# Kernel optimization log

Measured on AMD Instinct MI355X. Metric: run time of the kernel, lower is better.

The kernel has to match this reference:

```python
import jax, jax.numpy as jnp
import numpy as np

T, B, C = 1024, 16, 1024
H, K, PAD_L = 16, 7, 3  # num_heads, kernel_size, padding_l
OUT = 1024


def setup_inputs() -> dict:
    key = jax.random.key(0)
    ks = jax.random.split(key, 8)
    s_in = 1.0 / np.sqrt(C)
    return {
        "x": jax.random.normal(ks[0], (T, B, C), dtype=jnp.float32),
        "W1": jax.random.normal(ks[1], (C, C), dtype=jnp.float32) * s_in,
        "b1": jnp.zeros((C,), dtype=jnp.float32),
        "Wq": jax.random.normal(ks[2], (C, H * K), dtype=jnp.float32) * s_in,
        "bq": jnp.zeros((H * K,), dtype=jnp.float32),
        "conv_bias": jax.random.normal(ks[3], (C,), dtype=jnp.float32) * 0.02,
        "W2": jax.random.normal(ks[4], (C, OUT), dtype=jnp.float32) * s_in,
        "b2": jnp.zeros((OUT,), dtype=jnp.float32),
    }


def reference(x, W1, b1, Wq, bq, conv_bias, W2, b2):
    # linear1 (glu=False -> no activation)
    h = x @ W1 + b1                       # [T, B, C]
    Tn, Bn, Cn = h.shape
    R = Cn // H                           # channels per head
    # dynamic filter prediction from query (= h), softmax over K taps
    w = (h @ Wq + bq).reshape(Tn, Bn, H, K)
    w = jax.nn.softmax(w, axis=-1)        # [T, B, H, K]
    # unfold1d: pad PAD_L left, K-1-PAD_L right along time, gather K-windows
    hp = jnp.pad(h, ((PAD_L, K - 1 - PAD_L), (0, 0), (0, 0)))
    win = jnp.stack([hp[k:k + Tn] for k in range(K)], axis=-1)  # [T, B, C, K]
    win = win.reshape(Tn, Bn, H, R, K)
    out = jnp.einsum('tbhrk,tbhk->tbhr', win, w).reshape(Tn, Bn, Cn)
    out = out + conv_bias                 # [T, B, C]
    return out @ W2 + b2                  # [T, B, OUT]
```

## Files before the change

kernel.cpp:

```cpp
#include <hip/hip_runtime.h>
#include <math.h>

#define T_DIM 1024
#define B_DIM 16
#define C_DIM 1024
#define H_DIM 16
#define K_TAPS 7
#define PAD_LEFT 3
#define OUT_DIM 1024
#define M_DIM (T_DIM * B_DIM)
#define HK 112
#define HKP 128
#define KD 1024

typedef __attribute__((ext_vector_type(8))) short bf16x8;
typedef __attribute__((ext_vector_type(4))) float f32x4;

__device__ __forceinline__ ushort f2bf(float f) {
    union { float f; unsigned u; } v; v.f = f;
    unsigned u = v.u;
    u += 0x7fffu + ((u >> 16) & 1u);
    return (ushort)(u >> 16);
}
__device__ __forceinline__ float bf2f(ushort h) {
    union { unsigned u; float f; } v; v.u = ((unsigned)h) << 16;
    return v.f;
}

__global__ __launch_bounds__(256) void prep(const float* __restrict__ x,
                                            ushort* __restrict__ xb,
                                            const float* __restrict__ W1s,
                                            const float* __restrict__ Wqs,
                                            const float* __restrict__ W2s,
                                            ushort* __restrict__ W1t,
                                            ushort* __restrict__ Wqt,
                                            ushort* __restrict__ W2t) {
    __shared__ float tile[32][33];
    const int bx = blockIdx.x;
    if (bx < 8192) {
        int i = bx * 256 + threadIdx.x;
        const float4* p = (const float4*)x;
        float4 a = p[2 * i], b = p[2 * i + 1];
        uint4 o;
        o.x = (unsigned)f2bf(a.x) | ((unsigned)f2bf(a.y) << 16);
        o.y = (unsigned)f2bf(a.z) | ((unsigned)f2bf(a.w) << 16);
        o.z = (unsigned)f2bf(b.x) | ((unsigned)f2bf(b.y) << 16);
        o.w = (unsigned)f2bf(b.z) | ((unsigned)f2bf(b.w) << 16);
        ((uint4*)xb)[i] = o;
        return;
    }
    int tb  = bx - 8192;
    int nbx = tb % 68;
    int k0  = (tb / 68) * 32;
    const float* W; ushort* Wt; int N, Npad, nb;
    if (nbx < 32)      { W = W1s; Wt = W1t; N = 1024; Npad = 1024; nb = nbx; }
    else if (nbx < 36) { W = Wqs; Wt = Wqt; N = 112;  Npad = 128;  nb = nbx - 32; }
    else               { W = W2s; Wt = W2t; N = 1024; Npad = 1024; nb = nbx - 36; }
    int n0 = nb * 32;
    int tx = threadIdx.x & 31, ty = threadIdx.x >> 5;
#pragma unroll
    for (int j = 0; j < 4; ++j) {
        int k = k0 + ty * 4 + j;
        int n = n0 + tx;
        tile[ty * 4 + j][tx] = (n < N) ? W[(size_t)k * N + n] : 0.f;
    }
    __syncthreads();
#pragma unroll
    for (int j = 0; j < 4; ++j) {
        int n = n0 + ty * 4 + j;
        if (n < Npad)
            Wt[(size_t)n * KD + k0 + tx] = f2bf(tile[tx][ty * 4 + j]);
    }
}

#define PHASE(P2KS, MH, READB, STAGE_STMT, VM_STMT)                           \
    {                                                                         \
        if (READB) {                                                          \
            _Pragma("unroll")                                                 \
            for (int n = 0; n < 4; ++n)                                       \
                b[n] = *(const bf16x8*)(Bbase + (P2KS)*8192 + bOff + n*512);  \
        }                                                                     \
        bf16x8 a_[4];                                                         \
        _Pragma("unroll")                                                     \
        for (int m = 0; m < 4; ++m)                                           \
            a_[m] = *(const bf16x8*)(Abase + (P2KS)*8192 + aOff +             \
                                     (MH)*2048 + m*512);                      \
        STAGE_STMT;                                                           \
        VM_STMT;                                                              \
        __builtin_amdgcn_s_barrier();                                         \
        asm volatile("s_waitcnt lgkmcnt(0)" ::: "memory");                    \
        __builtin_amdgcn_sched_barrier(0);                                    \
        __builtin_amdgcn_s_setprio(1);                                        \
        _Pragma("unroll")                                                     \
        for (int m = 0; m < 4; ++m)                                           \
            _Pragma("unroll")                                                 \
            for (int n = 0; n < 4; ++n)                                       \
                acc[(MH)*4 + m][n] = __builtin_amdgcn_mfma_f32_16x16x32_bf16( \
                    a_[m], b[n], acc[(MH)*4 + m][n], 0, 0, 0);                \
        __builtin_amdgcn_s_setprio(0);                                        \
        __builtin_amdgcn_s_barrier();                                         \
        __builtin_amdgcn_sched_barrier(0);                                    \
    }

template <bool OUT_BF16>
__global__ __launch_bounds__(512, 1) void gemm8p(
    const ushort* __restrict__ A, const ushort* __restrict__ Bt,
    const float* __restrict__ bias, void* __restrict__ Cp, int ldc) {
    __shared__ ushort Lds[8 * 8192];

    const int tid  = threadIdx.x;
    const int lane = tid & 63;
    const int wid  = tid >> 6;
    const int wr = wid >> 2;
    const int wc = wid & 3;
    const int fr = lane & 15;
    const int fq = lane >> 4;

    const int orig = blockIdx.x;
    const int nid  = (orig & 7) * 32 + (orig >> 3);
    const int bm = (nid >> 2) * 256;
    const int bn = (nid & 3) * 256;

    const int srow = tid >> 2;
    const int scol = ((tid & 3) ^ ((tid >> 3) & 3)) * 8;
    const size_t sA = (size_t)(bm + srow) * KD + scol;
    const size_t sB = (size_t)(bn + srow) * KD + scol;
    const int sdst = wid * 64 * 8;

    const int slotSw = (fq ^ ((fr >> 1) & 3)) * 8;
    const int aOff = (wr * 128 + fr) * 32 + slotSw;
    const int bOff = (wc * 64 + fr) * 32 + slotSw;
    const ushort* Abase = &Lds[0];
    const ushort* Bbase = &Lds[4 * 8192];

    f32x4 acc[8][4];
#pragma unroll
    for (int m = 0; m < 8; ++m)
#pragma unroll
        for (int n = 0; n < 4; ++n) acc[m][n] = (f32x4){0.f, 0.f, 0.f, 0.f};

    auto stageA = [&](int slot, int koff) {
#pragma unroll
        for (int i = 0; i < 2; ++i)
            __builtin_amdgcn_global_load_lds(
                (const __attribute__((address_space(1))) void*)(A + sA + koff + (size_t)i * 128 * KD),
                (__attribute__((address_space(3))) void*)(&Lds[slot * 8192 + i * 4096 + sdst]),
                16, 0, 0);
    };
    auto stageB = [&](int slot, int koff) {
#pragma unroll
        for (int i = 0; i < 2; ++i)
            __builtin_amdgcn_global_load_lds(
                (const __attribute__((address_space(1))) void*)(Bt + sB + koff + (size_t)i * 128 * KD),
                (__attribute__((address_space(3))) void*)(&Lds[(4 + slot) * 8192 + i * 4096 + sdst]),
                16, 0, 0);
    };

    stageA(0, 0);   stageB(0, 0);
    stageA(1, 32);  stageB(1, 32);
    stageA(2, 64);  stageB(2, 64);
    stageA(3, 96);  stageB(3, 96);
    asm volatile("s_waitcnt vmcnt(12)" ::: "memory");
    __builtin_amdgcn_sched_barrier(0);
    __builtin_amdgcn_s_barrier();
    __builtin_amdgcn_sched_barrier(0);

#pragma unroll 1
    for (int j = 0; j < 8; ++j) {
        bf16x8 b[4];
        const int e = 2 * j;

        PHASE(0, 0, 1,
              { if (j >= 1) stageA(3, (e + 1) * 64 + 32); },
              { asm volatile("s_waitcnt vmcnt(6)" ::: "memory");
                __builtin_amdgcn_sched_barrier(0); })
        PHASE(0, 1, 0,
              { if (j >= 1) stageB(3, (e + 1) * 64 + 32); },
              (void)0; )
        PHASE(1, 0, 1,
              { if (j < 7) stageA(0, (e + 2) * 64); },
              { if (j == 7) { asm volatile("s_waitcnt vmcnt(4)" ::: "memory"); }
                else        { asm volatile("s_waitcnt vmcnt(6)" ::: "memory"); }
                __builtin_amdgcn_sched_barrier(0); })
        PHASE(1, 1, 0,
              { if (j < 7) stageB(0, (e + 2) * 64); },
              (void)0; )
        PHASE(2, 0, 1,
              { if (j < 7) stageA(1, (e + 2) * 64 + 32); },
              { if (j == 7) { asm volatile("s_waitcnt vmcnt(0)" ::: "memory"); }
                else        { asm volatile("s_waitcnt vmcnt(6)" ::: "memory"); }
                __builtin_amdgcn_sched_barrier(0); })
        PHASE(2, 1, 0,
              { if (j < 7) stageB(1, (e + 2) * 64 + 32); },
              (void)0; )
        PHASE(3, 0, 1,
              { if (j < 7) stageA(2, (e + 3) * 64); },
              { asm volatile("s_waitcnt vmcnt(6)" ::: "memory");
                __builtin_amdgcn_sched_barrier(0); })
        PHASE(3, 1, 0,
              { if (j < 7) stageB(2, (e + 3) * 64); },
              (void)0; )
    }

#pragma unroll
    for (int n = 0; n < 4; ++n) {
        int col = bn + wc * 64 + n * 16 + fr;
        float bv = bias[col];
#pragma unroll
        for (int m = 0; m < 8; ++m) {
#pragma unroll
            for (int r = 0; r < 4; ++r) {
                int row = bm + wr * 128 + m * 16 + fq * 4 + r;
                float v = acc[m][n][r] + bv;
                if (OUT_BF16)
                    ((ushort*)Cp)[(size_t)row * ldc + col] = f2bf(v);
                else
                    ((float*)Cp)[(size_t)row * ldc + col] = v;
            }
        }
    }
}

__global__ __launch_bounds__(256) void gemm_small(const ushort* __restrict__ A,
                                                  const ushort* __restrict__ Bt,
                                                  const float* __restrict__ bias,
                                                  float* __restrict__ Cp) {
    __shared__ ushort Als[64 * 32];
    __shared__ ushort Bls[128 * 32];
    const int tid  = threadIdx.x;
    const int lane = tid & 63;
    const int wid  = tid >> 6;
    const int wr = wid >> 1, wc = wid & 1;
    const int bm = blockIdx.y * 64;
    const int fq = lane >> 4, fr = lane & 15;

    f32x4 acc[2][4];
#pragma unroll
    for (int m = 0; m < 2; ++m)
#pragma unroll
        for (int n = 0; n < 4; ++n) acc[m][n] = (f32x4){0.f, 0.f, 0.f, 0.f};

    const int rA = tid >> 2, oA = (tid & 3) * 8;
    for (int k0 = 0; k0 < KD; k0 += 32) {
        __builtin_amdgcn_global_load_lds(
            (const __attribute__((address_space(1))) void*)&A[(size_t)(bm + rA) * KD + k0 + oA],
            (__attribute__((address_space(3))) void*)&Als[wid * 64 * 8], 16, 0, 0);
#pragma unroll
        for (int i = 0; i < 2; ++i) {
            int c = i * 256 + tid;
            __builtin_amdgcn_global_load_lds(
                (const __attribute__((address_space(1))) void*)&Bt[(size_t)(c >> 2) * KD + k0 + (c & 3) * 8],
                (__attribute__((address_space(3))) void*)&Bls[(i * 256 + wid * 64) * 8], 16, 0, 0);
        }
        __syncthreads();

        bf16x8 af[2], bfr[4];
#pragma unroll
        for (int m = 0; m < 2; ++m)
            af[m] = *(const bf16x8*)&Als[(wr * 32 + m * 16 + fr) * 32 + fq * 8];
#pragma unroll
        for (int n = 0; n < 4; ++n)
            bfr[n] = *(const bf16x8*)&Bls[(wc * 64 + n * 16 + fr) * 32 + fq * 8];
#pragma unroll
        for (int m = 0; m < 2; ++m)
#pragma unroll
            for (int n = 0; n < 4; ++n)
                acc[m][n] = __builtin_amdgcn_mfma_f32_16x16x32_bf16(
                    af[m], bfr[n], acc[m][n], 0, 0, 0);
        __syncthreads();
    }

#pragma unroll
    for (int m = 0; m < 2; ++m) {
#pragma unroll
        for (int n = 0; n < 4; ++n) {
            int col = wc * 64 + n * 16 + fr;
            if (col >= HK) continue;
            float bv = bias[col];
#pragma unroll
            for (int r = 0; r < 4; ++r) {
                int row = bm + wr * 32 + m * 16 + fq * 4 + r;
                Cp[(size_t)row * HK + col] = acc[m][n][r] + bv;
            }
        }
    }
}

__global__ __launch_bounds__(256) void dynconv2(const ushort* __restrict__ h,
                                                const float* __restrict__ q,
                                                const float* __restrict__ cbias,
                                                ushort* __restrict__ out) {
    __shared__ ushort hw[22][1024];
    __shared__ float wsm[16][HK];
    const int tid = threadIdx.x;
    const int b  = blockIdx.x & 15;
    const int t0 = (blockIdx.x >> 4) << 4;

    for (int i = tid; i < 22 * 128; i += 256) {
        int wrow = i >> 7;
        int c8   = (i & 127) * 8;
        int tt   = t0 + wrow - PAD_LEFT;
        uint4 v = make_uint4(0, 0, 0, 0);
        if (tt >= 0 && tt < T_DIM)
            v = *(const uint4*)&h[((size_t)tt * B_DIM + b) * C_DIM + c8];
        *(uint4*)&hw[wrow][c8] = v;
    }
    {
        int tl = tid >> 4, hh = tid & 15;
        int m = (t0 + tl) * B_DIM + b;
        const float* p = &q[(size_t)m * HK + hh * K_TAPS];
        float mx = p[0];
#pragma unroll
        for (int k = 1; k < K_TAPS; ++k) mx = fmaxf(mx, p[k]);
        float e[K_TAPS], s = 0.f;
#pragma unroll
        for (int k = 0; k < K_TAPS; ++k) { e[k] = __expf(p[k] - mx); s += e[k]; }
        float inv = 1.f / s;
#pragma unroll
        for (int k = 0; k < K_TAPS; ++k) wsm[tl][hh * K_TAPS + k] = e[k] * inv;
    }
    __syncthreads();

    const int c  = tid * 4;
    const int hh = c >> 6;
    float4 bias = *(const float4*)&cbias[c];

    for (int tl = 0; tl < 16; ++tl) {
        float a0 = bias.x, a1 = bias.y, a2 = bias.z, a3 = bias.w;
#pragma unroll
        for (int k = 0; k < K_TAPS; ++k) {
            ushort4 hv = *(const ushort4*)&hw[tl + k][c];
            float wk = wsm[tl][hh * K_TAPS + k];
            a0 = fmaf(bf2f(hv.x), wk, a0);
            a1 = fmaf(bf2f(hv.y), wk, a1);
            a2 = fmaf(bf2f(hv.z), wk, a2);
            a3 = fmaf(bf2f(hv.w), wk, a3);
        }
        ushort4 o;
        o.x = f2bf(a0); o.y = f2bf(a1); o.z = f2bf(a2); o.w = f2bf(a3);
        *(ushort4*)&out[((size_t)(t0 + tl) * B_DIM + b) * C_DIM + c] = o;
    }
}

extern "C" void kernel_launch(void* const* d_in, const int* in_sizes, int n_in,
                              void* d_out, int out_size, void* d_ws,
                              size_t ws_size, hipStream_t stream) {
    const float* x     = (const float*)d_in[0];
    const float* W1    = (const float*)d_in[1];
    const float* b1    = (const float*)d_in[2];
    const float* Wq    = (const float*)d_in[3];
    const float* bq    = (const float*)d_in[4];
    const float* cbias = (const float*)d_in[5];
    const float* W2    = (const float*)d_in[6];
    const float* b2    = (const float*)d_in[7];
    float* out = (float*)d_out;

    ushort* xb    = (ushort*)d_ws;
    ushort* hb    = xb    + (size_t)M_DIM * C_DIM;
    ushort* convb = hb    + (size_t)M_DIM * C_DIM;
    ushort* W1t   = convb + (size_t)M_DIM * C_DIM;
    ushort* W2t   = W1t   + (size_t)C_DIM * C_DIM;
    ushort* Wqt   = W2t   + (size_t)C_DIM * OUT_DIM;
    float*  q     = (float*)(Wqt + (size_t)HKP * C_DIM);

    prep<<<dim3(8192 + 68 * 32), dim3(256), 0, stream>>>(
        x, xb, W1, Wq, W2, W1t, Wqt, W2t);

    gemm8p<true><<<dim3(256), dim3(512), 0, stream>>>(xb, W1t, b1, hb, C_DIM);

    gemm_small<<<dim3(1, M_DIM / 64), dim3(256), 0, stream>>>(hb, Wqt, bq, q);

    dynconv2<<<dim3(B_DIM * T_DIM / 16), dim3(256), 0, stream>>>(
        hb, q, cbias, convb);

    gemm8p<false><<<dim3(256), dim3(512), 0, stream>>>(convb, W2t, b2, out,
                                                       OUT_DIM);
}
```

Before: 149.2 us.

## Fuse filter-prediction GEMM into dynamic conv kernel using the staged LDS window

Removes the separate gemm_small launch and the q round-trip through global memory. Each dynconv block now computes its 16x112 filter logits with MFMA, reading the h rows already staged in LDS and streaming Wq rows straight from global memory. It then applies the softmax in place in shared memory. The LDS row stride is padded to 1032 to avoid bank conflicts on the MFMA fragment reads. In exchange, every block re-reads Wqt (~224KB) from global/L2 and has less parallelism in the small GEMM.

Result: slower. 160.9 us (+7.8%).

```diff
diff --git a/kernel.cpp b/kernel.cpp
--- a/kernel.cpp
+++ b/kernel.cpp
@@ -12,6 +12,7 @@
 #define HK 112
 #define HKP 128
 #define KD 1024
+#define HWS 1032
 
 typedef __attribute__((ext_vector_type(8))) short bf16x8;
 typedef __attribute__((ext_vector_type(4))) float f32x4;
@@ -221,78 +222,18 @@
     }
 }
 
-__global__ __launch_bounds__(256) void gemm_small(const ushort* __restrict__ A,
-                                                  const ushort* __restrict__ Bt,
-                                                  const float* __restrict__ bias,
-                                                  float* __restrict__ Cp) {
-    __shared__ ushort Als[64 * 32];
-    __shared__ ushort Bls[128 * 32];
+__global__ __launch_bounds__(256) void dynconv3(const ushort* __restrict__ h,
+                                                const ushort* __restrict__ Wqt,
+                                                const float* __restrict__ bq,
+                                                const float* __restrict__ cbias,
+                                                ushort* __restrict__ out) {
+    __shared__ ushort hw[22 * HWS];
+    __shared__ float qs[16][HK];
     const int tid  = threadIdx.x;
     const int lane = tid & 63;
     const int wid  = tid >> 6;
-    const int wr = wid >> 1, wc = wid & 1;
-    const int bm = blockIdx.y * 64;
-    const int fq = lane >> 4, fr = lane & 15;
-
-    f32x4 acc[2][4];
-#pragma unroll
-    for (int m = 0; m < 2; ++m)
-#pragma unroll
-        for (int n = 0; n < 4; ++n) acc[m][n] = (f32x4){0.f, 0.f, 0.f, 0.f};
-
-    const int rA = tid >> 2, oA = (tid & 3) * 8;
-    for (int k0 = 0; k0 < KD; k0 += 32) {
-        __builtin_amdgcn_global_load_lds(
-            (const __attribute__((address_space(1))) void*)&A[(size_t)(bm + rA) * KD + k0 + oA],
-            (__attribute__((address_space(3))) void*)&Als[wid * 64 * 8], 16, 0, 0);
-#pragma unroll
-        for (int i = 0; i < 2; ++i) {
-            int c = i * 256 + tid;
-            __builtin_amdgcn_global_load_lds(
-                (const __attribute__((address_space(1))) void*)&Bt[(size_t)(c >> 2) * KD + k0 + (c & 3) * 8],
-                (__attribute__((address_space(3))) void*)&Bls[(i * 256 + wid * 64) * 8], 16, 0, 0);
-        }
-        __syncthreads();
-
-        bf16x8 af[2], bfr[4];
-#pragma unroll
-        for (int m = 0; m < 2; ++m)
-            af[m] = *(const bf16x8*)&Als[(wr * 32 + m * 16 + fr) * 32 + fq * 8];
-#pragma unroll
-        for (int n = 0; n < 4; ++n)
-            bfr[n] = *(const bf16x8*)&Bls[(wc * 64 + n * 16 + fr) * 32 + fq * 8];
-#pragma unroll
-        for (int m = 0; m < 2; ++m)
-#pragma unroll
-            for (int n = 0; n < 4; ++n)
-                acc[m][n] = __builtin_amdgcn_mfma_f32_16x16x32_bf16(
-                    af[m], bfr[n], acc[m][n], 0, 0, 0);
-        __syncthreads();
-    }
-
-#pragma unroll
-    for (int m = 0; m < 2; ++m) {
-#pragma unroll
-        for (int n = 0; n < 4; ++n) {
-            int col = wc * 64 + n * 16 + fr;
-            if (col >= HK) continue;
-            float bv = bias[col];
-#pragma unroll
-            for (int r = 0; r < 4; ++r) {
-                int row = bm + wr * 32 + m * 16 + fq * 4 + r;
-                Cp[(size_t)row * HK + col] = acc[m][n][r] + bv;
-            }
-        }
-    }
-}
-
-__global__ __launch_bounds__(256) void dynconv2(const ushort* __restrict__ h,
-                                                const float* __restrict__ q,
-                                                const float* __restrict__ cbias,
-                                                ushort* __restrict__ out) {
-    __shared__ ushort hw[22][1024];
-    __shared__ float wsm[16][HK];
-    const int tid = threadIdx.x;
+    const int fr = lane & 15;
+    const int fq = lane >> 4;
     const int b  = blockIdx.x & 15;
     const int t0 = (blockIdx.x >> 4) << 4;
 
@@ -303,12 +244,40 @@
         uint4 v = make_uint4(0, 0, 0, 0);
         if (tt >= 0 && tt < T_DIM)
             v = *(const uint4*)&h[((size_t)tt * B_DIM + b) * C_DIM + c8];
-        *(uint4*)&hw[wrow][c8] = v;
-    }
+        *(uint4*)&hw[wrow * HWS + c8] = v;
+    }
+    __syncthreads();
+
+    {
+        f32x4 acc0 = (f32x4){0.f, 0.f, 0.f, 0.f};
+        f32x4 acc1 = (f32x4){0.f, 0.f, 0.f, 0.f};
+        const int nf0 = wid * 2;
+        const int nf1 = wid * 2 + 1;
+        const ushort* aP  = &hw[(3 + fr) * HWS + fq * 8];
+        const ushort* b0P = &Wqt[(size_t)(nf0 * 16 + fr) * KD + fq * 8];
+        const ushort* b1P = &Wqt[(size_t)((nf1 < 7 ? nf1 : nf0) * 16 + fr) * KD + fq * 8];
+#pragma unroll 4
+        for (int k0 = 0; k0 < KD; k0 += 32) {
+            bf16x8 a  = *(const bf16x8*)(aP + k0);
+            bf16x8 v0 = *(const bf16x8*)(b0P + k0);
+            bf16x8 v1 = *(const bf16x8*)(b1P + k0);
+            acc0 = __builtin_amdgcn_mfma_f32_16x16x32_bf16(a, v0, acc0, 0, 0, 0);
+            acc1 = __builtin_amdgcn_mfma_f32_16x16x32_bf16(a, v1, acc1, 0, 0, 0);
+        }
+        float bv0 = bq[nf0 * 16 + fr];
+        float bv1 = (nf1 < 7) ? bq[nf1 * 16 + fr] : 0.f;
+#pragma unroll
+        for (int r = 0; r < 4; ++r) {
+            int row = fq * 4 + r;
+            qs[row][nf0 * 16 + fr] = acc0[r] + bv0;
+            if (nf1 < 7) qs[row][nf1 * 16 + fr] = acc1[r] + bv1;
+        }
+    }
+    __syncthreads();
+
     {
         int tl = tid >> 4, hh = tid & 15;
-        int m = (t0 + tl) * B_DIM + b;
-        const float* p = &q[(size_t)m * HK + hh * K_TAPS];
+        float* p = &qs[tl][hh * K_TAPS];
         float mx = p[0];
 #pragma unroll
         for (int k = 1; k < K_TAPS; ++k) mx = fmaxf(mx, p[k]);
@@ -317,7 +286,7 @@
         for (int k = 0; k < K_TAPS; ++k) { e[k] = __expf(p[k] - mx); s += e[k]; }
         float inv = 1.f / s;
 #pragma unroll
-        for (int k = 0; k < K_TAPS; ++k) wsm[tl][hh * K_TAPS + k] = e[k] * inv;
+        for (int k = 0; k < K_TAPS; ++k) p[k] = e[k] * inv;
     }
     __syncthreads();
 
@@ -329,8 +298,8 @@
         float a0 = bias.x, a1 = bias.y, a2 = bias.z, a3 = bias.w;
 #pragma unroll
         for (int k = 0; k < K_TAPS; ++k) {
-            ushort4 hv = *(const ushort4*)&hw[tl + k][c];
-            float wk = wsm[tl][hh * K_TAPS + k];
+            ushort4 hv = *(const ushort4*)&hw[(tl + k) * HWS + c];
+            float wk = qs[tl][hh * K_TAPS + k];
             a0 = fmaf(bf2f(hv.x), wk, a0);
             a1 = fmaf(bf2f(hv.y), wk, a1);
             a2 = fmaf(bf2f(hv.z), wk, a2);
@@ -361,17 +330,14 @@
     ushort* W1t   = convb + (size_t)M_DIM * C_DIM;
     ushort* W2t   = W1t   + (size_t)C_DIM * C_DIM;
     ushort* Wqt   = W2t   + (size_t)C_DIM * OUT_DIM;
-    float*  q     = (float*)(Wqt + (size_t)HKP * C_DIM);
 
     prep<<<dim3(8192 + 68 * 32), dim3(256), 0, stream>>>(
         x, xb, W1, Wq, W2, W1t, Wqt, W2t);
 
     gemm8p<true><<<dim3(256), dim3(512), 0, stream>>>(xb, W1t, b1, hb, C_DIM);
 
-    gemm_small<<<dim3(1, M_DIM / 64), dim3(256), 0, stream>>>(hb, Wqt, bq, q);
-
-    dynconv2<<<dim3(B_DIM * T_DIM / 16), dim3(256), 0, stream>>>(
-        hb, q, cbias, convb);
+    dynconv3<<<dim3(B_DIM * T_DIM / 16), dim3(256), 0, stream>>>(
+        hb, Wqt, bq, cbias, convb);
 
     gemm8p<false><<<dim3(256), dim3(512), 0, stream>>>(convb, W2t, b2, out,
                                                        OUT_DIM);
```
